# Kernel optimization log

Hardware: AMD Instinct MI355X
Metric: run time of the kernel (lower is better)

The kernel has to match this reference:

```python
import jax, jax.numpy as jnp
import numpy as np
import math

B, F, NB, H1, H2, K = 16384, 64, 64, 128, 128, 3
LN_EPS = 1e-5


def setup_inputs() -> dict:
    key = jax.random.key(0)
    ks = jax.random.split(key, 16)
    x = jax.random.normal(ks[0], (B, F), dtype=jnp.float32)
    # RBF params (per feature): centers init linspace(-3,3), log_widths = log(step)
    centers = jnp.broadcast_to(jnp.linspace(-3.0, 3.0, NB), (F, NB)).astype(jnp.float32)
    step = 6.0 / (NB - 1)
    log_widths = jnp.full((F, NB), math.log(step), dtype=jnp.float32)
    def lin(k, shape, fan_in):
        return jax.random.normal(k, shape, dtype=jnp.float32) / np.sqrt(fan_in)
    W1 = lin(ks[1], (F, NB, H1), NB); b1 = jnp.zeros((F, H1), jnp.float32)
    g1 = jnp.ones((F, H1), jnp.float32); be1 = jnp.zeros((F, H1), jnp.float32)
    W2 = lin(ks[2], (F, H1, H2), H1); b2 = jnp.zeros((F, H2), jnp.float32)
    g2 = jnp.ones((F, H2), jnp.float32); be2 = jnp.zeros((F, H2), jnp.float32)
    Wr = lin(ks[3], (F, NB, H2), NB); br = jnp.zeros((F, H2), jnp.float32)
    att = jnp.zeros((F,), jnp.float32)
    bias = jnp.zeros((H2,), jnp.float32)
    Wpi = lin(ks[4], (H2, K), H2); bpi = jnp.zeros((K,), jnp.float32)
    Wa = lin(ks[5], (H2, K), H2); ba = jnp.zeros((K,), jnp.float32)
    Wb = lin(ks[6], (H2, K), H2); bb = jnp.zeros((K,), jnp.float32)
    return dict(x=x, centers=centers, log_widths=log_widths, W1=W1, b1=b1, g1=g1,
                be1=be1, W2=W2, b2=b2, g2=g2, be2=be2, Wr=Wr, br=br, att=att,
                bias=bias, Wpi=Wpi, bpi=bpi, Wa=Wa, ba=ba, Wb=Wb, bb=bb)


def _layernorm(h, g, b):
    mu = jnp.mean(h, axis=-1, keepdims=True)
    var = jnp.mean((h - mu) ** 2, axis=-1, keepdims=True)
    return (h - mu) * jax.lax.rsqrt(var + LN_EPS) * g + b


def reference(x, centers, log_widths, W1, b1, g1, be1, W2, b2, g2, be2, Wr, br,
              att, bias, Wpi, bpi, Wa, ba, Wb, bb):
    # RBF expansion, feature axis batched: x [B,F] -> [B,F,NB]
    xc = jnp.clip(x, -10.0, 10.0)
    widths = jnp.exp(jnp.clip(log_widths, -5.0, 5.0)) + 0.1  # [F,NB]
    dist = (xc[:, :, None] - centers[None]) / widths[None]
    rbf = jnp.exp(-0.5 * jnp.clip(dist, -10.0, 10.0) ** 2)  # [B,F,NB]
    # per-feature MLP (grouped GEMMs via einsum)
    h = jnp.einsum('bfn,fnh->bfh', rbf, W1) + b1[None]
    h = jax.nn.gelu(_layernorm(h, g1[None], be1[None]), approximate=False)
    h = jnp.einsum('bfh,fhk->bfk', h, W2) + b2[None]
    h = jax.nn.gelu(_layernorm(h, g2[None], be2[None]), approximate=False)
    res = jnp.einsum('bfn,fnh->bfh', rbf, Wr) + br[None]
    stacked = h + 0.1 * res  # [B,F,H2]
    # attention-weighted aggregation over features
    w = jax.nn.softmax(att)
    agg = jnp.einsum('bfh,f->bh', stacked, w) + bias  # [B,H2]
    # mixture-beta head
    pi = jax.nn.softmax(agg @ Wpi + bpi, axis=-1)
    alpha = jnp.clip(jax.nn.softplus(agg @ Wa + ba) + 1.01, 1.01, 100.0)
    beta = jnp.clip(jax.nn.softplus(agg @ Wb + bb) + 1.01, 1.01, 100.0)
    pred = jnp.sum(pi * (alpha / (alpha + beta)), axis=-1)
    return jnp.clip(pred, 0.001, 0.999)
```

## Files before the change

### kernel.cpp

```cpp
#include <hip/hip_runtime.h>
#include <math.h>

#define BQ   16384
#define FQ   64
#define NBQ  64
#define HD   128
#define FG   4
#define FPG  16

typedef __attribute__((ext_vector_type(8))) short s16x8;
typedef __attribute__((ext_vector_type(4))) float f32x4;

__device__ __forceinline__ unsigned short f2bf(float x) {
    unsigned int u = __float_as_uint(x);
    return (unsigned short)((u + 0x7FFFu + ((u >> 16) & 1u)) >> 16);
}
__device__ __forceinline__ unsigned short bftr(float x) {
    return (unsigned short)(__float_as_uint(x) >> 16);
}

__device__ __forceinline__ float softplus_stable(float v) {
    return (v > 0.0f) ? (v + log1pf(expf(-v))) : log1pf(expf(v));
}

__device__ __forceinline__ f32x4 gelu4(f32x4 v) {
    const f32x4 v2 = v * v;
    const f32x4 tt = v2 * (-0.07135481f) + (-1.5957691f);
    const f32x4 s  = v * tt;
    f32x4 r;
    r[0] = __fdividef(v[0], 1.0f + __expf(s[0]));
    r[1] = __fdividef(v[1], 1.0f + __expf(s[1]));
    r[2] = __fdividef(v[2], 1.0f + __expf(s[2]));
    r[3] = __fdividef(v[3], 1.0f + __expf(s[3]));
    return r;
}

__device__ __forceinline__ void load16_lds(const unsigned short* g, unsigned short* l) {
    __builtin_amdgcn_global_load_lds(
        (const __attribute__((address_space(1))) unsigned int*)(uintptr_t)g,
        (__attribute__((address_space(3))) unsigned int*)(uintptr_t)l,
        16, 0, 0);
}

__global__ void __launch_bounds__(256) prep_small(
    const float* __restrict__ att, const float* __restrict__ log_widths,
    const float* __restrict__ centers, const float* __restrict__ br,
    const float* __restrict__ bias,
    float* __restrict__ wsoft, float* __restrict__ crw, float* __restrict__ rbias)
{
    __shared__ float ws[64];
    const int t = threadIdx.x;
    if (t < 64) {
        float v = att[t];
        float m = v;
#pragma unroll
        for (int s = 32; s >= 1; s >>= 1) m = fmaxf(m, __shfl_xor(m, s, 64));
        float e = expf(v - m);
        float ssum = e;
#pragma unroll
        for (int s = 32; s >= 1; s >>= 1) ssum += __shfl_xor(ssum, s, 64);
        const float w = e / ssum;
        ws[t] = w;
        wsoft[t] = w;
    }
    __syncthreads();
    for (int i = t; i < FQ * NBQ; i += 256) {
        float lw = fminf(fmaxf(log_widths[i], -5.0f), 5.0f);
        const float rw = 1.0f / (expf(lw) + 0.1f);
        ((float2*)crw)[i] = make_float2(rw, -centers[i] * rw);
    }
    if (t < HD) {
        float s = bias[t];
        for (int f = 0; f < FQ; ++f) s += 0.1f * ws[f] * br[f * HD + t];
        rbias[t] = s;
    }
}

__global__ void __launch_bounds__(256) prep_pack(
    const float* __restrict__ b1, const float* __restrict__ g1, const float* __restrict__ be1,
    const float* __restrict__ b2, const float* __restrict__ g2, const float* __restrict__ be2,
    float* __restrict__ Pk)
{
    const int id = blockIdx.x * 256 + threadIdx.x;
    if (id >= FQ * HD) return;
    ((float4*)Pk)[id * 2]     = make_float4(b1[id], g1[id], be1[id], 0.0f);
    ((float4*)Pk)[id * 2 + 1] = make_float4(b2[id], g2[id], be2[id], 0.0f);
}

__global__ void __launch_bounds__(256) prep_swz(
    const float* __restrict__ W1, const float* __restrict__ Wr, const float* __restrict__ W2,
    unsigned short* __restrict__ W1s, unsigned short* __restrict__ Wrs,
    unsigned short* __restrict__ W2s)
{
    const int gid = blockIdx.x * 256 + threadIdx.x;
    const float* W; unsigned short* dst; int K, id;
    if (gid < 65536)       { W = W1; dst = W1s; K = 64;  id = gid; }
    else if (gid < 131072) { W = Wr; dst = Wrs; K = 64;  id = gid - 65536; }
    else                   { W = W2; dst = W2s; K = 128; id = gid - 131072; }
    const int KB = K >> 3;
    const int nn = id & 15;
    const int kb = (id >> 4) % KB;
    const int nt = ((id >> 4) / KB) & 7;
    const int f  = id / (KB * 16 * 8);
    const float* src = W + ((size_t)f * K + kb * 8) * HD + nt * 16 + nn;
    s16x8 o;
#pragma unroll
    for (int j = 0; j < 8; ++j) o[j] = (short)f2bf(src[(size_t)j * HD]);
    *(s16x8*)(dst + (size_t)f * K * HD + ((size_t)(nt * KB + kb) * 16 + nn) * 8) = o;
}

__global__ void __launch_bounds__(256) prep_xtr(const float* __restrict__ x,
                                                float* __restrict__ xT) {
    __shared__ float tile[64][65];
    const int t  = threadIdx.x;
    const int b0 = blockIdx.x * 64;
    {
        const int row = t & 63, cg = (t >> 6) * 16;
        const float4* src = (const float4*)(x + (size_t)(b0 + row) * FQ + cg);
#pragma unroll
        for (int i = 0; i < 4; ++i) {
            const float4 v = src[i];
            tile[row][cg + i * 4 + 0] = v.x;
            tile[row][cg + i * 4 + 1] = v.y;
            tile[row][cg + i * 4 + 2] = v.z;
            tile[row][cg + i * 4 + 3] = v.w;
        }
    }
    __syncthreads();
    {
        const int f = t >> 2, r0 = (t & 3) * 16;
        float* dst = xT + (size_t)f * BQ + b0 + r0;
#pragma unroll
        for (int i = 0; i < 16; ++i) dst[i] = tile[r0 + i][f];
    }
}

__global__ void __launch_bounds__(256, 3) nam_main(
    const float* __restrict__ crw,
    const float* __restrict__ xT,
    const unsigned short* __restrict__ W1s,
    const unsigned short* __restrict__ Wrs,
    const unsigned short* __restrict__ W2s,
    const float* __restrict__ Pk,
    const float* __restrict__ wsoft,
    float* __restrict__ agg)
{
    __shared__ __align__(16) unsigned short wbuf[16384];
    __shared__ __align__(16) unsigned short hbuf[64 * 136];

    const int t    = threadIdx.x;
    const int ln   = t & 63;
    const int wv   = t >> 6;
    const int n    = ln & 15;
    const int q    = ln >> 4;
    const int wrow = wv * 16;
    const int fg   = blockIdx.x & 3;
    const int rb   = blockIdx.x >> 2;
    const int b0   = rb * 64;

    f32x4 acc[8];
#pragma unroll
    for (int nt = 0; nt < 8; ++nt) acc[nt] = f32x4{0.f, 0.f, 0.f, 0.f};

    for (int ff = 0; ff < FPG; ++ff) {
        const int f = fg * FPG + ((ff + rb) & (FPG - 1));
        __syncthreads();

        {
            const unsigned short* gw1 = W1s + (size_t)f * 8192;
            const unsigned short* gwr = Wrs + (size_t)f * 8192;
#pragma unroll
            for (int i = 0; i < 8; ++i) {
                const int chunk = i * 4 + wv;
                const unsigned short* src = (chunk < 16) ? (gw1 + chunk * 512)
                                                         : (gwr + (chunk - 16) * 512);
                load16_lds(src + ln * 8, wbuf + chunk * 512);
            }
        }

        {
            const int row = t & 63;
            const int ng  = t >> 6;
            const float xv = xT[(size_t)f * BQ + b0 + row];
            const float4* c4 = (const float4*)(crw + ((size_t)f * NBQ + ng * 16) * 2);
            float e[16];
#pragma unroll
            for (int i2 = 0; i2 < 8; ++i2) {
                const float4 cc = c4[i2];
                const float d0 = fmaf(xv, cc.x, cc.y);
                const float d1 = fmaf(xv, cc.z, cc.w);
                e[i2 * 2]     = __expf(-0.5f * d0 * d0);
                e[i2 * 2 + 1] = __expf(-0.5f * d1 * d1);
            }
            unsigned int p[8];
#pragma unroll
            for (int i2 = 0; i2 < 8; ++i2)
                p[i2] = __builtin_amdgcn_perm(__float_as_uint(e[2 * i2 + 1]),
                                              __float_as_uint(e[2 * i2]), 0x07060302u);
            *(int4*)&hbuf[row * 136 + ng * 16]     = make_int4(p[0], p[1], p[2], p[3]);
            *(int4*)&hbuf[row * 136 + ng * 16 + 8] = make_int4(p[4], p[5], p[6], p[7]);
        }
        __syncthreads();

        const s16x8 a0 = *(const s16x8*)&hbuf[(wrow + n) * 136 + q * 8];
        const s16x8 a1 = *(const s16x8*)&hbuf[(wrow + n) * 136 + 32 + q * 8];
        f32x4 hc[8], rc[8];
#pragma unroll
        for (int nt = 0; nt < 8; ++nt) {
            const s16x8 bA = *(const s16x8*)&wbuf[(nt * 8 + 0) * 128 + ln * 8];
            const s16x8 bB = *(const s16x8*)&wbuf[(nt * 8 + 4) * 128 + ln * 8];
            f32x4 z = f32x4{0.f, 0.f, 0.f, 0.f};
            z = __builtin_amdgcn_mfma_f32_16x16x32_bf16(a0, bA, z, 0, 0, 0);
            z = __builtin_amdgcn_mfma_f32_16x16x32_bf16(a1, bB, z, 0, 0, 0);
            hc[nt] = z;
            const s16x8 cA = *(const s16x8*)&wbuf[8192 + (nt * 8 + 0) * 128 + ln * 8];
            const s16x8 cB = *(const s16x8*)&wbuf[8192 + (nt * 8 + 4) * 128 + ln * 8];
            f32x4 y = f32x4{0.f, 0.f, 0.f, 0.f};
            y = __builtin_amdgcn_mfma_f32_16x16x32_bf16(a0, cA, y, 0, 0, 0);
            y = __builtin_amdgcn_mfma_f32_16x16x32_bf16(a1, cB, y, 0, 0, 0);
            rc[nt] = y;
        }
        __syncthreads();

        {
            const unsigned short* gw2 = W2s + (size_t)f * 16384;
#pragma unroll
            for (int i = 0; i < 8; ++i) {
                const int chunk = i * 4 + wv;
                load16_lds(gw2 + chunk * 512 + ln * 8, wbuf + chunk * 512);
            }
        }

        const size_t pkb = ((size_t)f * HD + n) * 8;
        f32x4 sm = {0.f, 0.f, 0.f, 0.f}, sq = {0.f, 0.f, 0.f, 0.f};
#pragma unroll
        for (int nt = 0; nt < 8; ++nt) {
            const float4 pA = *(const float4*)(Pk + pkb + nt * 128);
            const f32x4 v = hc[nt] + pA.x;
            hc[nt] = v; sm += v; sq += v * v;
        }
#pragma unroll
        for (int s = 1; s <= 8; s <<= 1) {
#pragma unroll
            for (int i = 0; i < 4; ++i) {
                sm[i] += __shfl_xor(sm[i], s, 64);
                sq[i] += __shfl_xor(sq[i], s, 64);
            }
        }
        f32x4 mu4 = sm * (1.0f / 128.0f);
        f32x4 var4 = sq * (1.0f / 128.0f) - mu4 * mu4;
        f32x4 rs4;
#pragma unroll
        for (int i = 0; i < 4; ++i) rs4[i] = rsqrtf(var4[i] + 1e-5f);
#pragma unroll
        for (int nt = 0; nt < 8; ++nt) {
            const float4 pA = *(const float4*)(Pk + pkb + nt * 128);
            const f32x4 sg = rs4 * pA.y;
            const f32x4 y  = (hc[nt] - mu4) * sg + pA.z;
            const f32x4 z  = gelu4(y);
            unsigned short* hp = hbuf + (wrow + q * 4) * 136 + nt * 16 + n;
            hp[0]   = bftr(z[0]);
            hp[136] = bftr(z[1]);
            hp[272] = bftr(z[2]);
            hp[408] = bftr(z[3]);
        }
        __syncthreads();

        s16x8 A2[4];
#pragma unroll
        for (int c = 0; c < 4; ++c)
            A2[c] = *(const s16x8*)&hbuf[(wrow + n) * 136 + c * 32 + q * 8];
        f32x4 h2[8];
#pragma unroll
        for (int nt = 0; nt < 8; ++nt) {
            f32x4 z = f32x4{0.f, 0.f, 0.f, 0.f};
#pragma unroll
            for (int c = 0; c < 4; ++c) {
                const s16x8 bF = *(const s16x8*)&wbuf[(nt * 16 + c * 4) * 128 + ln * 8];
                z = __builtin_amdgcn_mfma_f32_16x16x32_bf16(A2[c], bF, z, 0, 0, 0);
            }
            h2[nt] = z;
        }

        sm = f32x4{0.f, 0.f, 0.f, 0.f}; sq = f32x4{0.f, 0.f, 0.f, 0.f};
#pragma unroll
        for (int nt = 0; nt < 8; ++nt) {
            const float4 pB = *(const float4*)(Pk + pkb + nt * 128 + 4);
            const f32x4 v = h2[nt] + pB.x;
            h2[nt] = v; sm += v; sq += v * v;
        }
#pragma unroll
        for (int s = 1; s <= 8; s <<= 1) {
#pragma unroll
            for (int i = 0; i < 4; ++i) {
                sm[i] += __shfl_xor(sm[i], s, 64);
                sq[i] += __shfl_xor(sq[i], s, 64);
            }
        }
        mu4 = sm * (1.0f / 128.0f);
        var4 = sq * (1.0f / 128.0f) - mu4 * mu4;
#pragma unroll
        for (int i = 0; i < 4; ++i) rs4[i] = rsqrtf(var4[i] + 1e-5f);
        const float wf   = wsoft[f];
        const float wf01 = 0.1f * wf;
#pragma unroll
        for (int nt = 0; nt < 8; ++nt) {
            const float4 pB = *(const float4*)(Pk + pkb + nt * 128 + 4);
            const f32x4 sg = rs4 * pB.y;
            const f32x4 y  = (h2[nt] - mu4) * sg + pB.z;
            acc[nt] = gelu4(y) * wf + acc[nt];
            acc[nt] = rc[nt] * wf01 + acc[nt];
        }
    }

    float* ap = agg + (size_t)(b0 + wrow + q * 4) * HD + n;
#pragma unroll
    for (int nt = 0; nt < 8; ++nt) {
#pragma unroll
        for (int i = 0; i < 4; ++i) {
            atomicAdd(ap + (size_t)i * HD + nt * 16, acc[nt][i]);
        }
    }
}

__global__ void __launch_bounds__(256) nam_head(
    const float* __restrict__ agg, const float* __restrict__ rbias,
    const float* __restrict__ Wpi, const float* __restrict__ bpi,
    const float* __restrict__ Wa,  const float* __restrict__ ba,
    const float* __restrict__ Wb,  const float* __restrict__ bb,
    float* __restrict__ out)
{
    const int gid  = blockIdx.x * blockDim.x + threadIdx.x;
    const int row  = gid >> 6;
    const int lane = threadIdx.x & 63;
    if (row >= BQ) return;

    const float2 p  = ((const float2*)(agg + (size_t)row * HD))[lane];
    const float2 rb = ((const float2*)rbias)[lane];
    const float ax = p.x + rb.x;
    const float ay = p.y + rb.y;

    const float2* wp = (const float2*)Wpi;
    const float2* wa = (const float2*)Wa;
    const float2* wb = (const float2*)Wb;
    const float2 p01 = wp[lane * 3], p23 = wp[lane * 3 + 1], p45 = wp[lane * 3 + 2];
    const float2 a01 = wa[lane * 3], a23 = wa[lane * 3 + 1], a45 = wa[lane * 3 + 2];
    const float2 b01 = wb[lane * 3], b23 = wb[lane * 3 + 1], b45 = wb[lane * 3 + 2];

    float ppi0 = ax * p01.x + ay * p23.y;
    float ppi1 = ax * p01.y + ay * p45.x;
    float ppi2 = ax * p23.x + ay * p45.y;
    float pa0  = ax * a01.x + ay * a23.y;
    float pa1  = ax * a01.y + ay * a45.x;
    float pa2  = ax * a23.x + ay * a45.y;
    float pb0  = ax * b01.x + ay * b23.y;
    float pb1  = ax * b01.y + ay * b45.x;
    float pb2  = ax * b23.x + ay * b45.y;

#pragma unroll
    for (int s = 32; s >= 1; s >>= 1) {
        ppi0 += __shfl_xor(ppi0, s, 64);
        ppi1 += __shfl_xor(ppi1, s, 64);
        ppi2 += __shfl_xor(ppi2, s, 64);
        pa0  += __shfl_xor(pa0,  s, 64);
        pa1  += __shfl_xor(pa1,  s, 64);
        pa2  += __shfl_xor(pa2,  s, 64);
        pb0  += __shfl_xor(pb0,  s, 64);
        pb1  += __shfl_xor(pb1,  s, 64);
        pb2  += __shfl_xor(pb2,  s, 64);
    }

    if (lane == 0) {
        const float z0 = ppi0 + bpi[0], z1 = ppi1 + bpi[1], z2 = ppi2 + bpi[2];
        const float mz = fmaxf(z0, fmaxf(z1, z2));
        const float e0 = expf(z0 - mz), e1 = expf(z1 - mz), e2 = expf(z2 - mz);
        const float es = e0 + e1 + e2;

        const float al0 = fminf(fmaxf(softplus_stable(pa0 + ba[0]) + 1.01f, 1.01f), 100.0f);
        const float al1 = fminf(fmaxf(softplus_stable(pa1 + ba[1]) + 1.01f, 1.01f), 100.0f);
        const float al2 = fminf(fmaxf(softplus_stable(pa2 + ba[2]) + 1.01f, 1.01f), 100.0f);
        const float bt0 = fminf(fmaxf(softplus_stable(pb0 + bb[0]) + 1.01f, 1.01f), 100.0f);
        const float bt1 = fminf(fmaxf(softplus_stable(pb1 + bb[1]) + 1.01f, 1.01f), 100.0f);
        const float bt2 = fminf(fmaxf(softplus_stable(pb2 + bb[2]) + 1.01f, 1.01f), 100.0f);

        const float pred = (e0 * (al0 / (al0 + bt0))
                          + e1 * (al1 / (al1 + bt1))
                          + e2 * (al2 / (al2 + bt2))) / es;
        out[row] = fminf(fmaxf(pred, 0.001f), 0.999f);
    }
}

extern "C" void kernel_launch(void* const* d_in, const int* in_sizes, int n_in,
                              void* d_out, int out_size, void* d_ws, size_t ws_size,
                              hipStream_t stream) {
    const float* x          = (const float*)d_in[0];
    const float* centers    = (const float*)d_in[1];
    const float* log_widths = (const float*)d_in[2];
    const float* W1   = (const float*)d_in[3];
    const float* b1   = (const float*)d_in[4];
    const float* g1   = (const float*)d_in[5];
    const float* be1  = (const float*)d_in[6];
    const float* W2   = (const float*)d_in[7];
    const float* b2   = (const float*)d_in[8];
    const float* g2   = (const float*)d_in[9];
    const float* be2  = (const float*)d_in[10];
    const float* Wr   = (const float*)d_in[11];
    const float* br   = (const float*)d_in[12];
    const float* att  = (const float*)d_in[13];
    const float* bias = (const float*)d_in[14];
    const float* Wpi  = (const float*)d_in[15];
    const float* bpi  = (const float*)d_in[16];
    const float* Wa   = (const float*)d_in[17];
    const float* ba   = (const float*)d_in[18];
    const float* Wb   = (const float*)d_in[19];
    const float* bb   = (const float*)d_in[20];

    char* ws = (char*)d_ws;
    float*          wsoft = (float*)(ws + 0);
    float*          rbias = (float*)(ws + 1024);
    float*          crw   = (float*)(ws + 8192);
    float*          Pk    = (float*)(ws + 65536);
    float*          xT    = (float*)(ws + 327680);
    unsigned short* W1s   = (unsigned short*)(ws + 4521984);
    unsigned short* Wrs   = (unsigned short*)(ws + 5570560);
    unsigned short* W2s   = (unsigned short*)(ws + 6619136);
    float*          agg   = (float*)(ws + 8716288);

    prep_small<<<1, 256, 0, stream>>>(att, log_widths, centers, br, bias,
                                      wsoft, crw, rbias);
    prep_pack<<<32, 256, 0, stream>>>(b1, g1, be1, b2, g2, be2, Pk);
    prep_swz<<<1024, 256, 0, stream>>>(W1, Wr, W2, W1s, Wrs, W2s);
    prep_xtr<<<256, 256, 0, stream>>>(x, xT);
    hipMemsetAsync(agg, 0, (size_t)BQ * HD * sizeof(float), stream);

    nam_main<<<256 * FG, 256, 0, stream>>>(crw, xT, W1s, Wrs, W2s, Pk, wsoft, agg);

    nam_head<<<BQ / 4, 256, 0, stream>>>(agg, rbias, Wpi, bpi, Wa, ba, Wb, bb,
                                         (float*)d_out);
}
```

Measured before the change: 455.3 us.

## Enlarge row tile to 128 with 512-thread blocks and register RBF operands

The main kernel now handles 128 batch rows per block with 8 waves, so each weight tile loaded into LDS serves twice as many rows. RBF values are computed straight into MFMA A-operand registers instead of going through LDS, and the residual accumulation is folded into acc right away, which frees the rc registers. LayerNorm row reductions switch from shuffles to DPP row ops, the hidden buffer uses an XOR swizzle instead of padding, and the two small prep kernels are merged into one launch. In exchange the block is larger and the LDS footprint grows, which may limit occupancy, and the DPP reduction pattern has to be correct for 16-lane groups.

```diff
diff --git a/kernel.cpp b/kernel.cpp
--- a/kernel.cpp
+++ b/kernel.cpp
@@ -7,6 +7,8 @@
 #define HD   128
 #define FG   4
 #define FPG  16
+#define MT   128
+#define NT   512
 
 typedef __attribute__((ext_vector_type(8))) short s16x8;
 typedef __attribute__((ext_vector_type(4))) float f32x4;
@@ -35,6 +37,19 @@
     return r;
 }
 
+__device__ __forceinline__ float dppsum16(float x) {
+    int t;
+    t = __builtin_amdgcn_update_dpp(0, __float_as_int(x), 0xB1,  0xF, 0xF, true);
+    x += __int_as_float(t);
+    t = __builtin_amdgcn_update_dpp(0, __float_as_int(x), 0x4E,  0xF, 0xF, true);
+    x += __int_as_float(t);
+    t = __builtin_amdgcn_update_dpp(0, __float_as_int(x), 0x125, 0xF, 0xF, true);
+    x += __int_as_float(t);
+    t = __builtin_amdgcn_update_dpp(0, __float_as_int(x), 0x129, 0xF, 0xF, true);
+    x += __int_as_float(t);
+    return x;
+}
+
 __device__ __forceinline__ void load16_lds(const unsigned short* g, unsigned short* l) {
     __builtin_amdgcn_global_load_lds(
         (const __attribute__((address_space(1))) unsigned int*)(uintptr_t)g,
@@ -42,49 +57,53 @@
         16, 0, 0);
 }
 
-__global__ void __launch_bounds__(256) prep_small(
+__device__ __forceinline__ int hofs(int row, int col) {
+    return row * 128 + (col ^ (((row >> 2) & 3) << 4));
+}
+
+__global__ void __launch_bounds__(256) prep_misc(
     const float* __restrict__ att, const float* __restrict__ log_widths,
     const float* __restrict__ centers, const float* __restrict__ br,
     const float* __restrict__ bias,
-    float* __restrict__ wsoft, float* __restrict__ crw, float* __restrict__ rbias)
-{
-    __shared__ float ws[64];
-    const int t = threadIdx.x;
-    if (t < 64) {
-        float v = att[t];
-        float m = v;
-#pragma unroll
-        for (int s = 32; s >= 1; s >>= 1) m = fmaxf(m, __shfl_xor(m, s, 64));
-        float e = expf(v - m);
-        float ssum = e;
-#pragma unroll
-        for (int s = 32; s >= 1; s >>= 1) ssum += __shfl_xor(ssum, s, 64);
-        const float w = e / ssum;
-        ws[t] = w;
-        wsoft[t] = w;
-    }
-    __syncthreads();
-    for (int i = t; i < FQ * NBQ; i += 256) {
-        float lw = fminf(fmaxf(log_widths[i], -5.0f), 5.0f);
-        const float rw = 1.0f / (expf(lw) + 0.1f);
-        ((float2*)crw)[i] = make_float2(rw, -centers[i] * rw);
-    }
-    if (t < HD) {
-        float s = bias[t];
-        for (int f = 0; f < FQ; ++f) s += 0.1f * ws[f] * br[f * HD + t];
-        rbias[t] = s;
-    }
-}
-
-__global__ void __launch_bounds__(256) prep_pack(
     const float* __restrict__ b1, const float* __restrict__ g1, const float* __restrict__ be1,
     const float* __restrict__ b2, const float* __restrict__ g2, const float* __restrict__ be2,
+    float* __restrict__ wsoft, float* __restrict__ crw2, float* __restrict__ rbias,
     float* __restrict__ Pk)
 {
-    const int id = blockIdx.x * 256 + threadIdx.x;
-    if (id >= FQ * HD) return;
-    ((float4*)Pk)[id * 2]     = make_float4(b1[id], g1[id], be1[id], 0.0f);
-    ((float4*)Pk)[id * 2 + 1] = make_float4(b2[id], g2[id], be2[id], 0.0f);
+    const int t = threadIdx.x;
+    if (blockIdx.x == 0) {
+        __shared__ float ws[64];
+        if (t < 64) {
+            float v = att[t];
+            float m = v;
+#pragma unroll
+            for (int s = 32; s >= 1; s >>= 1) m = fmaxf(m, __shfl_xor(m, s, 64));
+            float e = expf(v - m);
+            float ssum = e;
+#pragma unroll
+            for (int s = 32; s >= 1; s >>= 1) ssum += __shfl_xor(ssum, s, 64);
+            const float w = e / ssum;
+            ws[t] = w;
+            wsoft[t] = w;
+        }
+        __syncthreads();
+        for (int i = t; i < FQ * NBQ; i += 256) {
+            float lw = fminf(fmaxf(log_widths[i], -5.0f), 5.0f);
+            const float rw = 1.0f / (expf(lw) + 0.1f);
+            ((float2*)crw2)[i] = make_float2(rw, -centers[i] * rw);
+        }
+        if (t < HD) {
+            float s = bias[t];
+            for (int f = 0; f < FQ; ++f) s += 0.1f * ws[f] * br[f * HD + t];
+            rbias[t] = s;
+        }
+    } else {
+        const int id = (blockIdx.x - 1) * 256 + t;
+        if (id < FQ * HD) {
+            ((float4*)Pk)[id * 2]     = make_float4(b1[id], g1[id], be1[id], 0.0f);
+            ((float4*)Pk)[id * 2 + 1] = make_float4(b2[id], g2[id], be2[id], 0.0f);
+        }
+    }
 }
 
 __global__ void __launch_bounds__(256) prep_swz(
@@ -135,8 +154,8 @@
     }
 }
 
-__global__ void __launch_bounds__(256, 3) nam_main(
-    const float* __restrict__ crw,
+__global__ void __launch_bounds__(NT, 4) nam_main(
+    const float* __restrict__ crw2,
     const float* __restrict__ xT,
     const unsigned short* __restrict__ W1s,
     const unsigned short* __restrict__ Wrs,
@@ -146,7 +165,7 @@
     float* __restrict__ agg)
 {
     __shared__ __align__(16) unsigned short wbuf[16384];
-    __shared__ __align__(16) unsigned short hbuf[64 * 136];
+    __shared__ __align__(16) unsigned short hbuf[16384];
 
     const int t    = threadIdx.x;
     const int ln   = t & 63;
@@ -156,7 +175,7 @@
     const int wrow = wv * 16;
     const int fg   = blockIdx.x & 3;
     const int rb   = blockIdx.x >> 2;
-    const int b0   = rb * 64;
+    const int b0   = rb * MT;
 
     f32x4 acc[8];
 #pragma unroll
@@ -170,41 +189,43 @@
             const unsigned short* gw1 = W1s + (size_t)f * 8192;
             const unsigned short* gwr = Wrs + (size_t)f * 8192;
 #pragma unroll
-            for (int i = 0; i < 8; ++i) {
-                const int chunk = i * 4 + wv;
+            for (int i = 0; i < 4; ++i) {
+                const int chunk = i * 8 + wv;
                 const unsigned short* src = (chunk < 16) ? (gw1 + chunk * 512)
                                                          : (gwr + (chunk - 16) * 512);
                 load16_lds(src + ln * 8, wbuf + chunk * 512);
             }
         }
 
+        s16x8 a0, a1;
         {
-            const int row = t & 63;
-            const int ng  = t >> 6;
-            const float xv = xT[(size_t)f * BQ + b0 + row];
-            const float4* c4 = (const float4*)(crw + ((size_t)f * NBQ + ng * 16) * 2);
-            float e[16];
-#pragma unroll
-            for (int i2 = 0; i2 < 8; ++i2) {
-                const float4 cc = c4[i2];
-                const float d0 = fmaf(xv, cc.x, cc.y);
-                const float d1 = fmaf(xv, cc.z, cc.w);
-                e[i2 * 2]     = __expf(-0.5f * d0 * d0);
-                e[i2 * 2 + 1] = __expf(-0.5f * d1 * d1);
+            float xv = xT[(size_t)f * BQ + b0 + wrow + n];
+            xv = fminf(fmaxf(xv, -10.0f), 10.0f);
+            const float4* c4 = ((const float4*)crw2) + f * 32;
+            unsigned int p[8];
+#pragma unroll
+            for (int h = 0; h < 2; ++h) {
+#pragma unroll
+                for (int i = 0; i < 4; ++i) {
+                    const float4 cc = c4[h * 16 + q * 4 + i];
+                    const float d0 = fmaf(xv, cc.x, cc.y);
+                    const float d1 = fmaf(xv, cc.z, cc.w);
+                    const float e0 = __expf(-0.5f * d0 * d0);
+                    const float e1 = __expf(-0.5f * d1 * d1);
+                    p[h * 4 + i] = __builtin_amdgcn_perm(__float_as_uint(e1),
+                                                         __float_as_uint(e0), 0x07060302u);
+                }
             }
-            unsigned int p[8];
-#pragma unroll
-            for (int i2 = 0; i2 < 8; ++i2)
-                p[i2] = __builtin_amdgcn_perm(__float_as_uint(e[2 * i2 + 1]),
-                                              __float_as_uint(e[2 * i2]), 0x07060302u);
-            *(int4*)&hbuf[row * 136 + ng * 16]     = make_int4(p[0], p[1], p[2], p[3]);
-            *(int4*)&hbuf[row * 136 + ng * 16 + 8] = make_int4(p[4], p[5], p[6], p[7]);
-        }
+            int4 pa = make_int4(p[0], p[1], p[2], p[3]);
+            int4 pb = make_int4(p[4], p[5], p[6], p[7]);
+            a0 = *(s16x8*)&pa;
+            a1 = *(s16x8*)&pb;
+        }
+        const float wf   = wsoft[f];
+        const float wf01 = 0.1f * wf;
         __syncthreads();
 
-        const s16x8 a0 = *(const s16x8*)&hbuf[(wrow + n) * 136 + q * 8];
-        const s16x8 a1 = *(const s16x8*)&hbuf[(wrow + n) * 136 + 32 + q * 8];
-        f32x4 hc[8], rc[8];
+        f32x4 hc[8];
 #pragma unroll
         for (int nt = 0; nt < 8; ++nt) {
             const s16x8 bA = *(const s16x8*)&wbuf[(nt * 8 + 0) * 128 + ln * 8];
@@ -218,15 +239,15 @@
             f32x4 y = f32x4{0.f, 0.f, 0.f, 0.f};
             y = __builtin_amdgcn_mfma_f32_16x16x32_bf16(a0, cA, y, 0, 0, 0);
             y = __builtin_amdgcn_mfma_f32_16x16x32_bf16(a1, cB, y, 0, 0, 0);
-            rc[nt] = y;
+            acc[nt] = y * wf01 + acc[nt];
         }
         __syncthreads();
 
         {
             const unsigned short* gw2 = W2s + (size_t)f * 16384;
 #pragma unroll
-            for (int i = 0; i < 8; ++i) {
-                const int chunk = i * 4 + wv;
+            for (int i = 0; i < 4; ++i) {
+                const int chunk = i * 8 + wv;
                 load16_lds(gw2 + chunk * 512 + ln * 8, wbuf + chunk * 512);
             }
         }
@@ -239,37 +260,31 @@
             const f32x4 v = hc[nt] + pA.x;
             hc[nt] = v; sm += v; sq += v * v;
         }
-#pragma unroll
-        for (int s = 1; s <= 8; s <<= 1) {
-#pragma unroll
-            for (int i = 0; i < 4; ++i) {
-                sm[i] += __shfl_xor(sm[i], s, 64);
-                sq[i] += __shfl_xor(sq[i], s, 64);
-            }
-        }
-        f32x4 mu4 = sm * (1.0f / 128.0f);
-        f32x4 var4 = sq * (1.0f / 128.0f) - mu4 * mu4;
-        f32x4 rs4;
-#pragma unroll
-        for (int i = 0; i < 4; ++i) rs4[i] = rsqrtf(var4[i] + 1e-5f);
+        f32x4 mu4, rs4;
+#pragma unroll
+        for (int i = 0; i < 4; ++i) {
+            const float s  = dppsum16(sm[i]);
+            const float qq = dppsum16(sq[i]);
+            mu4[i] = s * (1.0f / 128.0f);
+            const float var = qq * (1.0f / 128.0f) - mu4[i] * mu4[i];
+            rs4[i] = rsqrtf(var + 1e-5f);
+        }
 #pragma unroll
         for (int nt = 0; nt < 8; ++nt) {
             const float4 pA = *(const float4*)(Pk + pkb + nt * 128);
             const f32x4 sg = rs4 * pA.y;
             const f32x4 y  = (hc[nt] - mu4) * sg + pA.z;
             const f32x4 z  = gelu4(y);
-            unsigned short* hp = hbuf + (wrow + q * 4) * 136 + nt * 16 + n;
-            hp[0]   = bftr(z[0]);
-            hp[136] = bftr(z[1]);
-            hp[272] = bftr(z[2]);
-            hp[408] = bftr(z[3]);
+#pragma unroll
+            for (int i = 0; i < 4; ++i)
+                hbuf[hofs(wrow + q * 4 + i, nt * 16 + n)] = bftr(z[i]);
         }
         __syncthreads();
 
         s16x8 A2[4];
 #pragma unroll
         for (int c = 0; c < 4; ++c)
-            A2[c] = *(const s16x8*)&hbuf[(wrow + n) * 136 + c * 32 + q * 8];
+            A2[c] = *(const s16x8*)&hbuf[hofs(wrow + n, c * 32 + q * 8)];
         f32x4 h2[8];
 #pragma unroll
         for (int nt = 0; nt < 8; ++nt) {
@@ -290,26 +305,19 @@
             h2[nt] = v; sm += v; sq += v * v;
         }
 #pragma unroll
-        for (int s = 1; s <= 8; s <<= 1) {
-#pragma unroll
-            for (int i = 0; i < 4; ++i) {
-                sm[i] += __shfl_xor(sm[i], s, 64);
-                sq[i] += __shfl_xor(sq[i], s, 64);
-            }
-        }
-        mu4 = sm * (1.0f / 128.0f);
-        var4 = sq * (1.0f / 128.0f) - mu4 * mu4;
-#pragma unroll
-        for (int i = 0; i < 4; ++i) rs4[i] = rsqrtf(var4[i] + 1e-5f);
-        const float wf   = wsoft[f];
-        const float wf01 = 0.1f * wf;
+        for (int i = 0; i < 4; ++i) {
+            const float s  = dppsum16(sm[i]);
+            const float qq = dppsum16(sq[i]);
+            mu4[i] = s * (1.0f / 128.0f);
+            const float var = qq * (1.0f / 128.0f) - mu4[i] * mu4[i];
+            rs4[i] = rsqrtf(var + 1e-5f);
+        }
 #pragma unroll
         for (int nt = 0; nt < 8; ++nt) {
             const float4 pB = *(const float4*)(Pk + pkb + nt * 128 + 4);
             const f32x4 sg = rs4 * pB.y;
             const f32x4 y  = (h2[nt] - mu4) * sg + pB.z;
             acc[nt] = gelu4(y) * wf + acc[nt];
-            acc[nt] = rc[nt] * wf01 + acc[nt];
         }
     }
 
@@ -418,7 +426,7 @@
     char* ws = (char*)d_ws;
     float*          wsoft = (float*)(ws + 0);
     float*          rbias = (float*)(ws + 1024);
-    float*          crw   = (float*)(ws + 8192);
+    float*          crw2  = (float*)(ws + 8192);
     float*          Pk    = (float*)(ws + 65536);
     float*          xT    = (float*)(ws + 327680);
     unsigned short* W1s   = (unsigned short*)(ws + 4521984);
@@ -426,14 +434,15 @@
     unsigned short* W2s   = (unsigned short*)(ws + 6619136);
     float*          agg   = (float*)(ws + 8716288);
 
-    prep_small<<<1, 256, 0, stream>>>(att, log_widths, centers, br, bias,
-                                      wsoft, crw, rbias);
-    prep_pack<<<32, 256, 0, stream>>>(b1, g1, be1, b2, g2, be2, Pk);
+    prep_misc<<<33, 256, 0, stream>>>(att, log_widths, centers, br, bias,
+                                      b1, g1, be1, b2, g2, be2,
+                                      wsoft, crw2, rbias, Pk);
     prep_swz<<<1024, 256, 0, stream>>>(W1, Wr, W2, W1s, Wrs, W2s);
     prep_xtr<<<256, 256, 0, stream>>>(x, xT);
     hipMemsetAsync(agg, 0, (size_t)BQ * HD * sizeof(float), stream);
 
-    nam_main<<<256 * FG, 256, 0, stream>>>(crw, xT, W1s, Wrs, W2s, Pk, wsoft, agg);
+    nam_main<<<(BQ / MT) * FG, NT, 0, stream>>>(crw2, xT, W1s, Wrs, W2s, Pk,
+                                                wsoft, agg);
 
     nam_head<<<BQ / 4, 256, 0, stream>>>(agg, rbias, Wpi, bpi, Wa, ba, Wb, bb,
                                          (float*)d_out);
```

New measurement: 434.2 us. -4.6%, faster.
